# Optimization experiments

Measured on AMD Instinct MI355X. Metric: run time of the kernel, lower is better.

The kernel has to match this reference:

```python
import jax, jax.numpy as jnp
import numpy as np

B, S, D, H, K = 16, 4096, 256, 512, 3
EPS = 1e-5


def setup_inputs() -> dict:
    key = jax.random.key(0)
    ks = jax.random.split(key, 16)
    glorot = lambda k, shape: jax.random.uniform(
        k, shape, jnp.float32, -1.0, 1.0) * np.sqrt(6.0 / (shape[0] + shape[-1]))
    return {
        "inputs": jax.random.normal(ks[0], (B, S, D), jnp.float32),
        "mask": jax.random.randint(ks[1], (B, S), 0, 2, jnp.int32),
        "in_w": glorot(ks[2], (H, D)),
        "in_b": jnp.zeros((H,), jnp.float32),
        "gate_w": glorot(ks[3], (H, D)),
        "gate_b": jnp.zeros((H,), jnp.float32),
        "dw_w": glorot(ks[4], (H, 1, K)),
        "dw_b": jnp.zeros((H,), jnp.float32),
        "pw_w": glorot(ks[5], (H, H, 1)),
        "pw_b": jnp.zeros((H,), jnp.float32),
        "ln_g": jnp.ones((H,), jnp.float32),
        "ln_b": jnp.zeros((H,), jnp.float32),
        "A_log": jax.random.normal(ks[6], (H,), jnp.float32) * -0.1,
        "Bp": jax.random.normal(ks[7], (H,), jnp.float32) * 0.1,
        "Cp": jax.random.normal(ks[8], (H,), jnp.float32) * 0.1,
    }


def _forward(inputs, mask, in_w, in_b, gate_w, gate_b, dw_w, dw_b,
             pw_w, pw_b, ln_g, ln_b, A_log, Bp, Cp):
    # projections: torch Linear is x @ W.T + b
    x_lin = jnp.einsum('bsd,hd->bsh', inputs, in_w) + in_b
    g_lin = jnp.einsum('bsd,hd->bsh', inputs, gate_w) + gate_b
    h = jnp.tanh(x_lin)
    m_f = mask.astype(h.dtype)                      # [B,S]
    h = h * m_f[:, :, None]
    # depthwise conv over time: [B,H,S] with groups=H, 'same' padding
    pad = (K - 1) // 2
    h_t = jnp.transpose(h, (0, 2, 1))               # [B,H,S]
    h_conv = jax.lax.conv_general_dilated(
        h_t, dw_w, window_strides=(1,), padding=[(pad, pad)],
        dimension_numbers=('NCH', 'OIH', 'NCH'), feature_group_count=H)
    h_conv = h_conv + dw_b[None, :, None]
    h_conv = jnp.transpose(h_conv, (0, 2, 1))       # [B,S,H]
    # pointwise 1x1 conv
    h_conv = jnp.einsum('bsh,oh->bso', h_conv, pw_w[:, :, 0]) + pw_b
    u = jax.nn.silu(h_conv + h)
    g = jax.nn.sigmoid(g_lin)
    a_exp = jnp.exp(-jax.nn.softplus(A_log))        # [H]

    def step(carry, xs):
        state, last = carry
        ut, gt, mt = xs                             # [B,H],[B,H],[B]
        new_state = gt * (a_exp * state) + (1.0 - gt) * (Bp * ut)
        keep = (mt > 0.5)[:, None]
        state = jnp.where(keep, new_state, state)
        y = state * Cp
        last = jnp.where(keep, y, last)
        return (state, last), last

    init = (jnp.zeros((B, H), u.dtype), jnp.zeros((B, H), u.dtype))
    xs = (jnp.transpose(u, (1, 0, 2)), jnp.transpose(g, (1, 0, 2)),
          jnp.transpose(m_f, (1, 0)))
    _, y_seq = jax.lax.scan(step, init, xs)         # [S,B,H]
    y_seq = jnp.transpose(y_seq, (1, 0, 2))         # [B,S,H]
    # LayerNorm over last dim
    mu = jnp.mean(y_seq, axis=-1, keepdims=True)
    var = jnp.var(y_seq, axis=-1, keepdims=True)
    return (y_seq - mu) * jax.lax.rsqrt(var + EPS) * ln_g + ln_b


def reference(inputs, mask, in_w, in_b, gate_w, gate_b, dw_w, dw_b,
              pw_w, pw_b, ln_g, ln_b, A_log, Bp, Cp):
    return _forward(inputs, mask, in_w, in_b, gate_w, gate_b, dw_w, dw_b,
                    pw_w, pw_b, ln_g, ln_b, A_log, Bp, Cp)
```

## Files before the change

kernel.cpp:

```cpp
#include <hip/hip_runtime.h>
#include <hip/hip_bf16.h>
#include <math.h>

#define B_  16
#define S_  4096
#define D_  256
#define H_  512
#define BS_ 65536
#define BSH_ 33554432L
#define BSD_ 16777216L
#define CCH 128
#define LCH 32
#define TPAD 136

typedef __bf16 bf16;
typedef __bf16 bf16x8 __attribute__((ext_vector_type(8)));
typedef float  f32x4  __attribute__((ext_vector_type(4)));

#define AS1 __attribute__((address_space(1)))
#define AS3 __attribute__((address_space(3)))

__device__ __forceinline__ void gload_lds16(const void* g, void* l) {
  __builtin_amdgcn_global_load_lds((const AS1 void*)g, (AS3 void*)l, 16, 0, 0);
}

#if __has_builtin(__builtin_amdgcn_exp2f)
#define EXP2F __builtin_amdgcn_exp2f
#else
#define EXP2F exp2f
#endif
#if __has_builtin(__builtin_amdgcn_rcpf)
#define RCPF __builtin_amdgcn_rcpf
#else
#define RCPF(x) (1.f/(x))
#endif
#define L2E 1.4426950408889634f

__device__ __forceinline__ float fsigmoid(float x) {
  return RCPF(1.f + EXP2F(-L2E * x));
}
__device__ __forceinline__ float ftanh(float x) {
  return 2.f * RCPF(1.f + EXP2F(-2.f * L2E * x)) - 1.f;
}
__device__ __forceinline__ float fsilu(float x) {
  return x * RCPF(1.f + EXP2F(-L2E * x));
}

__global__ void k_cast_x(const float* __restrict__ x, bf16* __restrict__ xb, int n8) {
  int i = blockIdx.x * blockDim.x + threadIdx.x;
  if (i >= n8) return;
  const float4* p = (const float4*)x + (long)i * 2;
  float4 a = p[0], b = p[1];
  bf16x8 o;
  o[0]=(bf16)a.x; o[1]=(bf16)a.y; o[2]=(bf16)a.z; o[3]=(bf16)a.w;
  o[4]=(bf16)b.x; o[5]=(bf16)b.y; o[6]=(bf16)b.z; o[7]=(bf16)b.w;
  ((bf16x8*)xb)[i] = o;
}

__global__ void k_cast_w(const float* __restrict__ in_w, const float* __restrict__ gate_w,
                         const float* __restrict__ pw_w,
                         bf16* __restrict__ w1, bf16* __restrict__ pw) {
  int i = blockIdx.x * blockDim.x + threadIdx.x;
  const int HD = H_ * D_;
  if (i < HD)            w1[i] = (bf16)in_w[i];
  else if (i < 2 * HD)   w1[i] = (bf16)gate_w[i - HD];
  else {
    int j = i - 2 * HD;
    if (j < H_ * H_)     pw[j] = (bf16)pw_w[j];
  }
}

template<int KDIM, int EPI>
__global__ __launch_bounds__(256)
void k_gemm(const bf16* __restrict__ A, const bf16* __restrict__ Bw,
            const int* __restrict__ mask,
            const float* __restrict__ bias0, const float* __restrict__ bias1,
            const bf16* __restrict__ hbuf,
            bf16* __restrict__ out0, bf16* __restrict__ out1, int Ntiles)
{
  extern __shared__ char smem_raw[];
  bf16* As_ = (bf16*)smem_raw;
  bf16* Bs_ = (bf16*)smem_raw + 8192;
  bf16* tile = (bf16*)smem_raw;

  const int t = threadIdx.x;
  const int w = t >> 6, lane = t & 63;
  const int nwg = gridDim.x;
  const int wg = (blockIdx.x & 7) * (nwg >> 3) + (blockIdx.x >> 3);
  const int bn0 = (wg % Ntiles) * 128;
  const int bm0 = (wg / Ntiles) * 128;
  const int wm = w >> 1, wn = w & 1;
  const int srow = t >> 2;
  const int skoff = (t & 3) * 8;
  const int fr = lane & 15, kq = lane >> 4;

  f32x4 acc[4][4];
#pragma unroll
  for (int i = 0; i < 4; ++i)
#pragma unroll
    for (int j = 0; j < 4; ++j) acc[i][j] = (f32x4){0.f, 0.f, 0.f, 0.f};

#pragma unroll
  for (int i = 0; i < 2; ++i) {
    gload_lds16(A  + (long)(bm0 + i * 64 + srow) * KDIM + skoff,
                As_ + i * 2048 + t * 8);
    gload_lds16(Bw + (long)(bn0 + i * 64 + srow) * KDIM + skoff,
                Bs_ + i * 2048 + t * 8);
  }

  int cur = 0;
  for (int k0 = 0; k0 < KDIM; k0 += 32) {
    __syncthreads();
    if (k0 + 32 < KDIM) {
      const int nxt = cur ^ 1;
#pragma unroll
      for (int i = 0; i < 2; ++i) {
        gload_lds16(A  + (long)(bm0 + i * 64 + srow) * KDIM + (k0 + 32) + skoff,
                    As_ + nxt * 4096 + i * 2048 + t * 8);
        gload_lds16(Bw + (long)(bn0 + i * 64 + srow) * KDIM + (k0 + 32) + skoff,
                    Bs_ + nxt * 4096 + i * 2048 + t * 8);
      }
    }
    const bf16* As = As_ + cur * 4096;
    const bf16* Bs = Bs_ + cur * 4096;
    bf16x8 af[4], bfr[4];
#pragma unroll
    for (int mi = 0; mi < 4; ++mi)
      af[mi] = *(const bf16x8*)&As[(wm * 64 + mi * 16 + fr) * 32 + kq * 8];
#pragma unroll
    for (int ni = 0; ni < 4; ++ni)
      bfr[ni] = *(const bf16x8*)&Bs[(wn * 64 + ni * 16 + fr) * 32 + kq * 8];
#pragma unroll
    for (int mi = 0; mi < 4; ++mi)
#pragma unroll
      for (int ni = 0; ni < 4; ++ni)
        acc[mi][ni] = __builtin_amdgcn_mfma_f32_16x16x32_bf16(af[mi], bfr[ni], acc[mi][ni], 0, 0, 0);
    cur ^= 1;
  }
  __syncthreads();

  const bool hside = (EPI != 1) || (bn0 < H_);
#pragma unroll
  for (int mi = 0; mi < 4; ++mi) {
#pragma unroll
    for (int rr = 0; rr < 4; ++rr) {
      const int row = wm * 64 + mi * 16 + kq * 4 + rr;
      const int gm = bm0 + row;
      float mf = 1.f;
      if (EPI == 1) mf = (mask[gm] != 0) ? 1.f : 0.f;
#pragma unroll
      for (int ni = 0; ni < 4; ++ni) {
        const int col = wn * 64 + ni * 16 + fr;
        float c = acc[mi][ni][rr];
        float val;
        if (EPI == 1) {
          const int gn = bn0 + col;
          val = hside ? ftanh(c + bias0[gn]) * mf
                      : fsigmoid(c + bias1[gn - H_]);
        } else {
          val = c + bias0[bn0 + col];
        }
        tile[row * TPAD + col] = (bf16)val;
      }
    }
  }
  __syncthreads();

  const int pr = t >> 4;
  const int pc = (t & 15) * 8;
#pragma unroll
  for (int rr = 0; rr < 8; ++rr) {
    const int row = pr + rr * 16;
    const long gm = bm0 + row;
    bf16x8 v = *(const bf16x8*)&tile[row * TPAD + pc];
    if (EPI == 1) {
      if (hside) *(bf16x8*)&out0[gm * H_ + bn0 + pc] = v;
      else       *(bf16x8*)&out1[gm * H_ + (bn0 - H_) + pc] = v;
    } else {
      bf16x8 hb = *(const bf16x8*)&hbuf[gm * H_ + bn0 + pc];
      bf16x8 o;
#pragma unroll
      for (int k = 0; k < 8; ++k) {
        float s = (float)v[k] + (float)hb[k];
        o[k] = (bf16)fsilu(s);
      }
      *(bf16x8*)&out0[gm * H_ + bn0 + pc] = o;
    }
  }
}

__global__ void k_dwconv(const bf16* __restrict__ h, const float* __restrict__ dww,
                         const float* __restrict__ dwb, bf16* __restrict__ hc)
{
  long idx = (long)blockIdx.x * blockDim.x + threadIdx.x;
  long m = idx >> 6;
  int h8 = ((int)idx & 63) << 3;
  int s = (int)(m & (S_ - 1));
  bf16x8 c0, c1, c2;
#pragma unroll
  for (int j = 0; j < 8; ++j) { c0[j] = (bf16)0.f; c2[j] = (bf16)0.f; }
  if (s > 0)        c0 = *(const bf16x8*)(h + (m - 1) * H_ + h8);
  c1 = *(const bf16x8*)(h + m * H_ + h8);
  if (s < S_ - 1)   c2 = *(const bf16x8*)(h + (m + 1) * H_ + h8);
  bf16x8 o;
#pragma unroll
  for (int j = 0; j < 8; ++j) {
    int hh = h8 + j;
    float v = (float)c0[j] * dww[hh * 3 + 0] + (float)c1[j] * dww[hh * 3 + 1]
            + (float)c2[j] * dww[hh * 3 + 2] + dwb[hh];
    o[j] = (bf16)v;
  }
  *(bf16x8*)(hc + m * H_ + h8) = o;
}


__global__ __launch_bounds__(512)
void k_scan1(const bf16* __restrict__ u, const bf16* __restrict__ g,
             const int* __restrict__ mask, const float* __restrict__ A_log,
             const float* __restrict__ Bp,
             float* __restrict__ Ac, float* __restrict__ Bc)
{
  int c = blockIdx.x, b = blockIdx.y, h = threadIdx.x;
  float aexp = 1.f / (1.f + expf(A_log[h]));
  float bp = Bp[h];
  float At = 1.f, Bt = 0.f;
  long base = ((long)b * S_ + (long)c * LCH) * H_ + h;
  const int* mrow = mask + b * S_ + c * LCH;
  for (int sl = 0; sl < LCH; ++sl) {
    float uv = (float)u[base + (long)sl * H_];
    float gv = (float)g[base + (long)sl * H_];
    bool mm = mrow[sl] != 0;
    float a_s = mm ? gv * aexp : 1.f;
    float b_s = mm ? (1.f - gv) * (bp * uv) : 0.f;
    At = a_s * At;
    Bt = fmaf(a_s, Bt, b_s);
  }
  long o = ((long)c * B_ + b) * H_ + h;
  Ac[o] = At; Bc[o] = Bt;
}

__global__ __launch_bounds__(256)
void k_scan2(const float* __restrict__ Ac, const float* __restrict__ Bc,
             float* __restrict__ Sin)
{
  int tid = blockIdx.x * 256 + threadIdx.x;
  int b = tid >> 9, h = tid & (H_ - 1);
  const long stride = (long)B_ * H_;
  long o = (long)b * H_ + h;
  float st = 0.f;
  float a = Ac[o], bb = Bc[o];
  for (int c = 0; c < CCH; ++c) {
    float an = 0.f, bn = 0.f;
    if (c + 1 < CCH) { an = Ac[o + stride]; bn = Bc[o + stride]; }
    Sin[o] = st;
    st = fmaf(a, st, bb);
    a = an; bb = bn; o += stride;
  }
}

__global__ __launch_bounds__(512)
void k_scan3(const bf16* __restrict__ u, const bf16* __restrict__ g,
             const int* __restrict__ mask, const float* __restrict__ A_log,
             const float* __restrict__ Bp, const float* __restrict__ Cp,
             const float* __restrict__ Sin,
             const float* __restrict__ ln_g, const float* __restrict__ ln_b,
             float* __restrict__ out)
{
  __shared__ float ylds[LCH][H_];
  int c = blockIdx.x, b = blockIdx.y, h = threadIdx.x;
  float aexp = 1.f / (1.f + expf(A_log[h]));
  float bp = Bp[h], cp = Cp[h];
  float st = Sin[((long)c * B_ + b) * H_ + h];
  long base = ((long)b * S_ + (long)c * LCH) * H_ + h;
  const int* mrow = mask + b * S_ + c * LCH;
  for (int sl = 0; sl < LCH; ++sl) {
    float uv = (float)u[base + (long)sl * H_];
    float gv = (float)g[base + (long)sl * H_];
    bool mm = mrow[sl] != 0;
    float a_s = mm ? gv * aexp : 1.f;
    float b_s = mm ? (1.f - gv) * (bp * uv) : 0.f;
    st = fmaf(a_s, st, b_s);
    ylds[sl][h] = st * cp;
  }
  __syncthreads();
  int wv = h >> 6, ln = h & 63;
#pragma unroll
  for (int rr = 0; rr < 4; ++rr) {
    int row = wv * 4 + rr;
    float v[8];
    float sum = 0.f, sq = 0.f;
#pragma unroll
    for (int j = 0; j < 8; ++j) {
      v[j] = ylds[row][ln + 64 * j];
      sum += v[j]; sq += v[j] * v[j];
    }
#pragma unroll
    for (int off = 32; off; off >>= 1) {
      sum += __shfl_xor(sum, off);
      sq  += __shfl_xor(sq, off);
    }
    float mu = sum * (1.f / H_);
    float var = sq * (1.f / H_) - mu * mu;
    float rs = rsqrtf(var + 1e-5f);
    long ob = ((long)b * S_ + (long)c * LCH + row) * H_;
#pragma unroll
    for (int j = 0; j < 8; ++j) {
      int col = ln + 64 * j;
      out[ob + col] = (v[j] - mu) * rs * ln_g[col] + ln_b[col];
    }
  }
}

extern "C" void kernel_launch(void* const* d_in, const int* in_sizes, int n_in,
                              void* d_out, int out_size, void* d_ws, size_t ws_size,
                              hipStream_t stream)
{
  const float* x      = (const float*)d_in[0];
  const int*   mask   = (const int*)d_in[1];
  const float* in_w   = (const float*)d_in[2];
  const float* in_b   = (const float*)d_in[3];
  const float* gate_w = (const float*)d_in[4];
  const float* gate_b = (const float*)d_in[5];
  const float* dw_w   = (const float*)d_in[6];
  const float* dw_b   = (const float*)d_in[7];
  const float* pw_w   = (const float*)d_in[8];
  const float* pw_b   = (const float*)d_in[9];
  const float* ln_g   = (const float*)d_in[10];
  const float* ln_b   = (const float*)d_in[11];
  const float* A_log  = (const float*)d_in[12];
  const float* Bp     = (const float*)d_in[13];
  const float* Cp     = (const float*)d_in[14];

  char* ws = (char*)d_ws;
  bf16*  xb  = (bf16*)(ws + 0L);
  bf16*  h   = (bf16*)(ws + 33554432L);
  bf16*  hc  = (bf16*)(ws + 100663296L);
  bf16*  u   = (bf16*)(ws + 167772160L);
  bf16*  g   = (bf16*)(ws + 234881024L);
  bf16*  w1  = (bf16*)(ws + 301989888L);
  bf16*  pw  = (bf16*)(ws + 302514176L);
  float* Ac  = (float*)(ws + 303038464L);
  float* Bc  = (float*)(ws + 307232768L);
  float* Sin = (float*)(ws + 311427072L);
  float* out = (float*)d_out;

  const int gemm_lds = 128 * TPAD * 2;

  k_cast_x<<<8192, 256, 0, stream>>>(x, xb, (int)(BSD_ / 8));
  k_cast_w<<<2048, 256, 0, stream>>>(in_w, gate_w, pw_w, w1, pw);
  k_gemm<256, 1><<<512 * 8, 256, gemm_lds, stream>>>(xb, w1, mask, in_b, gate_b, nullptr, h, g, 8);
  k_dwconv<<<16384, 256, 0, stream>>>(h, dw_w, dw_b, hc);
  k_gemm<512, 2><<<512 * 4, 256, gemm_lds, stream>>>(hc, pw, nullptr, pw_b, nullptr, h, u, nullptr, 4);
  k_scan1<<<dim3(CCH, B_), 512, 0, stream>>>(u, g, mask, A_log, Bp, Ac, Bc);
  k_scan2<<<32, 256, 0, stream>>>(Ac, Bc, Sin);
  k_scan3<<<dim3(CCH, B_), 512, 0, stream>>>(u, g, mask, A_log, Bp, Cp, Sin, ln_g, ln_b, out);
}
```

Baseline: 383.7 us.

## Triple-buffer GEMM LDS loads with explicit vmcnt waits and deeper prefetch

Turns the bf16 MFMA GEMM's double-buffered global-to-LDS pipeline into a three-stage ring, prefetching two K-tiles ahead. Explicit s_waitcnt vmcnt counts replace the full __syncthreads, so a wave only waits for the stage it is about to consume. A second barrier after the fragment reads lets the next stage be issued before the MFMAs. The intent is to hide more global-load latency behind compute. In exchange, per-block LDS grows to 48KB, which may lower occupancy, and there is now an extra barrier per K-step.

After: 373.6 us. -2.6%, faster.

```diff
diff --git a/kernel.cpp b/kernel.cpp
--- a/kernel.cpp
+++ b/kernel.cpp
@@ -80,7 +80,7 @@
 {
   extern __shared__ char smem_raw[];
   bf16* As_ = (bf16*)smem_raw;
-  bf16* Bs_ = (bf16*)smem_raw + 8192;
+  bf16* Bs_ = (bf16*)smem_raw + 3 * 4096;
   bf16* tile = (bf16*)smem_raw;
 
   const int t = threadIdx.x;
@@ -93,6 +93,7 @@
   const int srow = t >> 2;
   const int skoff = (t & 3) * 8;
   const int fr = lane & 15, kq = lane >> 4;
+  constexpr int NT = KDIM / 32;
 
   f32x4 acc[4][4];
 #pragma unroll
@@ -100,29 +101,29 @@
 #pragma unroll
     for (int j = 0; j < 4; ++j) acc[i][j] = (f32x4){0.f, 0.f, 0.f, 0.f};
 
-#pragma unroll
-  for (int i = 0; i < 2; ++i) {
-    gload_lds16(A  + (long)(bm0 + i * 64 + srow) * KDIM + skoff,
-                As_ + i * 2048 + t * 8);
-    gload_lds16(Bw + (long)(bn0 + i * 64 + srow) * KDIM + skoff,
-                Bs_ + i * 2048 + t * 8);
-  }
-
-  int cur = 0;
-  for (int k0 = 0; k0 < KDIM; k0 += 32) {
-    __syncthreads();
-    if (k0 + 32 < KDIM) {
-      const int nxt = cur ^ 1;
-#pragma unroll
-      for (int i = 0; i < 2; ++i) {
-        gload_lds16(A  + (long)(bm0 + i * 64 + srow) * KDIM + (k0 + 32) + skoff,
-                    As_ + nxt * 4096 + i * 2048 + t * 8);
-        gload_lds16(Bw + (long)(bn0 + i * 64 + srow) * KDIM + (k0 + 32) + skoff,
-                    Bs_ + nxt * 4096 + i * 2048 + t * 8);
-      }
-    }
-    const bf16* As = As_ + cur * 4096;
-    const bf16* Bs = Bs_ + cur * 4096;
+#define STAGE(tt)                                                              \
+  {                                                                            \
+    const int _bi = (tt) % 3;                                                  \
+    _Pragma("unroll")                                                          \
+    for (int i = 0; i < 2; ++i) {                                              \
+      gload_lds16(A  + (long)(bm0 + i * 64 + srow) * KDIM + (tt) * 32 + skoff, \
+                  As_ + _bi * 4096 + i * 2048 + t * 8);                        \
+      gload_lds16(Bw + (long)(bn0 + i * 64 + srow) * KDIM + (tt) * 32 + skoff, \
+                  Bs_ + _bi * 4096 + i * 2048 + t * 8);                        \
+    }                                                                          \
+  }
+
+  STAGE(0); STAGE(1); STAGE(2);
+
+#pragma unroll
+  for (int kt = 0; kt < NT; ++kt) {
+    if (kt + 2 < NT)      asm volatile("s_waitcnt vmcnt(8)" ::: "memory");
+    else if (kt + 1 < NT) asm volatile("s_waitcnt vmcnt(4)" ::: "memory");
+    else                  asm volatile("s_waitcnt vmcnt(0)" ::: "memory");
+    __builtin_amdgcn_s_barrier();
+
+    const bf16* As = As_ + (kt % 3) * 4096;
+    const bf16* Bs = Bs_ + (kt % 3) * 4096;
     bf16x8 af[4], bfr[4];
 #pragma unroll
     for (int mi = 0; mi < 4; ++mi)
@@ -130,14 +131,19 @@
 #pragma unroll
     for (int ni = 0; ni < 4; ++ni)
       bfr[ni] = *(const bf16x8*)&Bs[(wn * 64 + ni * 16 + fr) * 32 + kq * 8];
+
+    asm volatile("s_waitcnt lgkmcnt(0)" ::: "memory");
+    __builtin_amdgcn_s_barrier();
+
+    if (kt + 3 < NT) STAGE(kt + 3);
+
 #pragma unroll
     for (int mi = 0; mi < 4; ++mi)
 #pragma unroll
       for (int ni = 0; ni < 4; ++ni)
         acc[mi][ni] = __builtin_amdgcn_mfma_f32_16x16x32_bf16(af[mi], bfr[ni], acc[mi][ni], 0, 0, 0);
-    cur ^= 1;
-  }
-  __syncthreads();
+  }
+#undef STAGE
 
   const bool hside = (EPI != 1) || (bn0 < H_);
 #pragma unroll
@@ -344,7 +350,7 @@
   float* Sin = (float*)(ws + 311427072L);
   float* out = (float*)d_out;
 
-  const int gemm_lds = 128 * TPAD * 2;
+  const int gemm_lds = 3 * 2 * 8192;
 
   k_cast_x<<<8192, 256, 0, stream>>>(x, xb, (int)(BSD_ / 8));
   k_cast_w<<<2048, 256, 0, stream>>>(in_w, gate_w, pw_w, w1, pw);
```
